# Kernel tuning notes

Measured on AMD Instinct MI355X. Metric: run time of the kernel, lower is better.

## Reference

```python
import jax, jax.numpy as jnp
import numpy as np

B, S, D = 2, 2048, 2048
E, F, TOP_K = 16, 768, 2
NORM_TOPK_PROB = True


def setup_inputs() -> dict:
    key = jax.random.key(0)
    ks = jax.random.split(key, 5)
    sc = 0.02
    return {
        "hidden_states": jax.random.normal(ks[0], (B, S, D), jnp.float32),
        "router_w": jax.random.normal(ks[1], (E, D), jnp.float32) * sc,
        "gate_w": jax.random.normal(ks[2], (E, F, D), jnp.float32) * sc,
        "up_w": jax.random.normal(ks[3], (E, F, D), jnp.float32) * sc,
        "down_w": jax.random.normal(ks[4], (E, D, F), jnp.float32) * sc,
    }


def reference(hidden_states, router_w, gate_w, up_w, down_w):
    b, s, d = hidden_states.shape
    x = hidden_states.reshape(-1, d)                      # [T, D]
    T = x.shape[0]
    # Router: logits, softmax in fp32, top-k
    router_logits = x @ router_w.T                        # [T, E]
    probs = jax.nn.softmax(router_logits.astype(jnp.float32), axis=-1)
    topk_w, topk_idx = jax.lax.top_k(probs, TOP_K)        # [T, K]
    if NORM_TOPK_PROB:
        topk_w = topk_w / jnp.sum(topk_w, axis=-1, keepdims=True)
    topk_w = topk_w.astype(x.dtype)
    # Combine weights as a dense [T, E] matrix (0 for unselected experts);
    # math-equivalent to the per-expert gather/index_add in the original.
    combine = jnp.zeros((T, E), x.dtype).at[jnp.arange(T)[:, None], topk_idx].add(topk_w)
    # Per-expert SwiGLU MLP on all tokens (zero-weight tokens contribute nothing)
    g = jax.nn.silu(jnp.einsum('td,efd->etf', x, gate_w))  # [E, T, F]
    u = jnp.einsum('td,efd->etf', x, up_w)                 # [E, T, F]
    h = (g * u) * combine.T[:, :, None]                    # weight before down-proj
    out = jnp.einsum('etf,edf->td', h, down_w)             # [T, D]
    return out.reshape(b, s, d), router_logits
```

## Files before the change

### kernel.cpp

```cpp
#include <hip/hip_runtime.h>
#include <stdint.h>


#define NTOK 4096
#define DIM  2048
#define NEXP 16
#define FDIM 768
#define BK   32

#define WS_CNT     0
#define WS_CUR     256
#define WS_NTILES  512
#define WS_TILE_E  576
#define WS_TILE_B  736
#define WS_TOKE    1024
#define WS_TOKW    9216
#define WS_SLOTT   17408
#define SLOTW_NEW  27648
#define SLOTW_OLD  26624
#define WS_TOKSLOT 40960
#define MAX_TILES  144

#define TMN 128
#define TNA 64
#define TNB 128
#define MAX_SLOTS_N 10240
#define MAX_TILES_N 80
#define TMO 64
#define MAX_SLOTS_O 9216

#define B_XBF  262144ull
#define B_H    (B_XBF + (size_t)NTOK*DIM*2)
#define B_GBF  (B_H + (size_t)MAX_SLOTS_N*FDIM*2)
#define B_UBF  (B_GBF + (size_t)NEXP*FDIM*DIM*2)
#define B_DBF  (B_UBF + (size_t)NEXP*FDIM*DIM*2)
#define WS_NEED (B_DBF + (size_t)NEXP*FDIM*DIM*2)
#define B_OSL  B_GBF
#define B_HOLD 143360ull

typedef __attribute__((ext_vector_type(8))) short short8;
typedef __attribute__((ext_vector_type(4))) float f32x4;

__device__ __forceinline__ unsigned short f2bf(float f) {
    unsigned u = __float_as_uint(f);
    return (unsigned short)((u + 0x7FFFu + ((u >> 16) & 1u)) >> 16);
}

__device__ __forceinline__ short8 cvt8(float4 v0, float4 v1) {
    short8 s;
    s[0] = (short)f2bf(v0.x); s[1] = (short)f2bf(v0.y);
    s[2] = (short)f2bf(v0.z); s[3] = (short)f2bf(v0.w);
    s[4] = (short)f2bf(v1.x); s[5] = (short)f2bf(v1.y);
    s[6] = (short)f2bf(v1.z); s[7] = (short)f2bf(v1.w);
    return s;
}

__device__ __forceinline__ void gl_lds16(const void* g, void* l) {
    __builtin_amdgcn_global_load_lds(
        (const __attribute__((address_space(1))) unsigned int*)g,
        (__attribute__((address_space(3))) unsigned int*)l, 16, 0, 0);
}

__global__ __launch_bounds__(256) void cvtw_k(
    const float* __restrict__ g, const float* __restrict__ u, const float* __restrict__ d,
    unsigned short* __restrict__ go, unsigned short* __restrict__ uo,
    unsigned short* __restrict__ dd, int n8)
{
    int i = blockIdx.x * 256 + threadIdx.x;
    if (i >= n8) return;
    const float* s;
    unsigned short* o;
    if (blockIdx.y == 0)      { s = g; o = go; }
    else if (blockIdx.y == 1) { s = u; o = uo; }
    else                      { s = d; o = dd; }
    const float4* p = (const float4*)(s + (size_t)i * 8);
    *(short8*)(o + (size_t)i * 8) = cvt8(p[0], p[1]);
}

__global__ __launch_bounds__(256) void router_k(
    const float* __restrict__ x, const float* __restrict__ rw,
    float* __restrict__ logits_out, int* __restrict__ wsi, float* __restrict__ wsf,
    unsigned short* __restrict__ xbf)
{
    int wid = threadIdx.x >> 6, lane = threadIdx.x & 63;
    int t = blockIdx.x * 4 + wid;
    const float* xr = x + (size_t)t * DIM;

    float acc[NEXP];
#pragma unroll
    for (int e = 0; e < NEXP; e++) acc[e] = 0.f;
    for (int i = 0; i < DIM / 64; i++) {
        float xv = xr[i * 64 + lane];
        if (xbf) xbf[(size_t)t * DIM + i * 64 + lane] = f2bf(xv);
#pragma unroll
        for (int e = 0; e < NEXP; e++) acc[e] += xv * rw[e * DIM + i * 64 + lane];
    }
#pragma unroll
    for (int e = 0; e < NEXP; e++) {
        float v = acc[e];
        for (int off = 32; off; off >>= 1) v += __shfl_down(v, off);
        acc[e] = v;
    }
    if (lane == 0) {
#pragma unroll
        for (int e = 0; e < NEXP; e++) logits_out[t * NEXP + e] = acc[e];
        int i0 = 0; float m0 = acc[0];
#pragma unroll
        for (int e = 1; e < NEXP; e++) if (acc[e] > m0) { m0 = acc[e]; i0 = e; }
        int i1 = -1; float m1 = -3.4e38f;
#pragma unroll
        for (int e = 0; e < NEXP; e++) if (e != i0 && acc[e] > m1) { m1 = acc[e]; i1 = e; }
        float w0 = 1.f / (1.f + __expf(m1 - m0));
        wsi[WS_TOKE + t * 2 + 0] = i0;
        wsi[WS_TOKE + t * 2 + 1] = i1;
        wsf[WS_TOKW + t * 2 + 0] = w0;
        wsf[WS_TOKW + t * 2 + 1] = 1.f - w0;
        atomicAdd(&wsi[WS_CNT + i0 * 16], 1);
        atomicAdd(&wsi[WS_CNT + i1 * 16], 1);
    }
}

__global__ void scan_k(int* __restrict__ wsi, float* __restrict__ wsf,
                       int tm, int slotw, int max_slots)
{
    if (threadIdx.x == 0) {
        int total = 0, tiles = 0;
        for (int e = 0; e < NEXP; e++) {
            int c = wsi[WS_CNT + e * 16];
            int nt = (c + tm - 1) / tm;
            wsi[WS_CNT + e * 16] = total;
            for (int j = 0; j < nt; j++) {
                wsi[WS_TILE_E + tiles] = e;
                wsi[WS_TILE_B + tiles] = total + j * tm;
                tiles++;
            }
            total += nt * tm;
        }
        wsi[WS_NTILES] = tiles;
    }
    for (int s = threadIdx.x; s < max_slots; s += blockDim.x) {
        wsi[WS_SLOTT + s] = 0;
        wsf[slotw + s] = 0.f;
    }
}

__global__ __launch_bounds__(256) void scatter_k(int* __restrict__ wsi,
                                                 float* __restrict__ wsf, int slotw)
{
    int t = blockIdx.x * blockDim.x + threadIdx.x;
    if (t >= NTOK) return;
#pragma unroll
    for (int k = 0; k < 2; k++) {
        int e = wsi[WS_TOKE + t * 2 + k];
        float w = wsf[WS_TOKW + t * 2 + k];
        int pos = atomicAdd(&wsi[WS_CUR + e * 16], 1);
        int s = wsi[WS_CNT + e * 16] + pos;
        wsi[WS_SLOTT + s] = t;
        wsf[slotw + s] = w;
        wsi[WS_TOKSLOT + t * 2 + k] = s;
    }
}


__global__ __launch_bounds__(256) void expertA_k(
    const unsigned short* __restrict__ xbf,
    const unsigned short* __restrict__ gbf,
    const unsigned short* __restrict__ ubf,
    const int* __restrict__ wsi, const float* __restrict__ wsf,
    unsigned short* __restrict__ H)
{
    __shared__ union {
        struct {
            unsigned short A[2][TMN * BK];
            unsigned short G[2][TNA * BK];
            unsigned short U[2][TNA * BK];
        } st;
        unsigned short Hs[TMN][TNA + 8];
    } sh;
    __shared__ int   Ts[TMN];
    __shared__ float Wl[TMN];

    int tile = blockIdx.y;
    if (tile >= wsi[WS_NTILES]) return;
    int e     = wsi[WS_TILE_E + tile];
    int slot0 = wsi[WS_TILE_B + tile];
    int f0    = blockIdx.x * TNA;
    int tid   = threadIdx.x;

    if (tid < TMN) {
        Ts[tid] = wsi[WS_SLOTT + slot0 + tid];
        Wl[tid] = wsf[SLOTW_NEW + slot0 + tid];
    }
    __syncthreads();

    int r0 = tid >> 2, seg = tid & 3;
    const unsigned short* ap0 = xbf + (size_t)Ts[r0] * DIM + seg * 8;
    const unsigned short* ap1 = xbf + (size_t)Ts[64 + r0] * DIM + seg * 8;
    const unsigned short* gp  = gbf + ((size_t)e * FDIM + f0 + r0) * DIM + seg * 8;
    const unsigned short* up  = ubf + ((size_t)e * FDIM + f0 + r0) * DIM + seg * 8;

    int wid = tid >> 6, lane = tid & 63;
    int wm = (wid >> 1) * 64, wn = (wid & 1) * 32;
    int lr = lane & 15, lk = (lane >> 4) * 8;

    f32x4 accg[4][2], accu[4][2];
#pragma unroll
    for (int i = 0; i < 4; i++)
#pragma unroll
        for (int j = 0; j < 2; j++) { accg[i][j] = (f32x4)0.f; accu[i][j] = (f32x4)0.f; }

    auto stage = [&](int b, int k0) {
        gl_lds16(ap0 + k0, &sh.st.A[b][(size_t)tid * 8]);
        gl_lds16(ap1 + k0, &sh.st.A[b][(size_t)(256 + tid) * 8]);
        gl_lds16(gp + k0,  &sh.st.G[b][(size_t)tid * 8]);
        gl_lds16(up + k0,  &sh.st.U[b][(size_t)tid * 8]);
    };
    auto comp = [&](int b) {
        short8 a[4], g[2], u[2];
#pragma unroll
        for (int mi = 0; mi < 4; mi++)
            a[mi] = *(const short8*)&sh.st.A[b][(wm + mi * 16 + lr) * BK + lk];
#pragma unroll
        for (int nj = 0; nj < 2; nj++) {
            g[nj] = *(const short8*)&sh.st.G[b][(wn + nj * 16 + lr) * BK + lk];
            u[nj] = *(const short8*)&sh.st.U[b][(wn + nj * 16 + lr) * BK + lk];
        }
#pragma unroll
        for (int mi = 0; mi < 4; mi++)
#pragma unroll
            for (int nj = 0; nj < 2; nj++) {
                accg[mi][nj] = __builtin_amdgcn_mfma_f32_16x16x32_bf16(a[mi], g[nj], accg[mi][nj], 0, 0, 0);
                accu[mi][nj] = __builtin_amdgcn_mfma_f32_16x16x32_bf16(a[mi], u[nj], accu[mi][nj], 0, 0, 0);
            }
    };

    stage(0, 0);
    __syncthreads();
    for (int k0 = 0; k0 < DIM; k0 += 2 * BK) {
        if (k0 + BK < DIM) stage(1, k0 + BK);
        comp(0);
        __syncthreads();
        if (k0 + 2 * BK < DIM) stage(0, k0 + 2 * BK);
        comp(1);
        __syncthreads();
    }

#pragma unroll
    for (int mi = 0; mi < 4; mi++)
#pragma unroll
        for (int nj = 0; nj < 2; nj++)
#pragma unroll
            for (int r = 0; r < 4; r++) {
                int m = wm + mi * 16 + (lane >> 4) * 4 + r;
                int n = wn + nj * 16 + lr;
                float g = accg[mi][nj][r];
                float u = accu[mi][nj][r];
                float sg = g / (1.f + __expf(-g));
                sh.Hs[m][n] = f2bf(sg * u * Wl[m]);
            }
    __syncthreads();

    int row = tid >> 1, cb = (tid & 1) * 32;
    unsigned short* dst = H + (size_t)(slot0 + row) * FDIM + f0 + cb;
#pragma unroll
    for (int c = 0; c < 4; c++)
        *(short8*)(dst + c * 8) = *(const short8*)&sh.Hs[row][cb + c * 8];
}

__global__ __launch_bounds__(256) void expertB_k(
    const unsigned short* __restrict__ H, const unsigned short* __restrict__ dbf,
    const int* __restrict__ wsi, float* __restrict__ O)
{
    __shared__ unsigned short As[2][TMN * BK];
    __shared__ unsigned short Bs[2][TNB * BK];

    int tile = blockIdx.y;
    if (tile >= wsi[WS_NTILES]) return;
    int e     = wsi[WS_TILE_E + tile];
    int slot0 = wsi[WS_TILE_B + tile];
    int d0    = blockIdx.x * TNB;
    int tid   = threadIdx.x;

    int r0 = tid >> 2, seg = tid & 3;
    const unsigned short* ap0 = H + (size_t)(slot0 + r0) * FDIM + seg * 8;
    const unsigned short* ap1 = H + (size_t)(slot0 + 64 + r0) * FDIM + seg * 8;
    const unsigned short* bp0 = dbf + ((size_t)e * DIM + d0 + r0) * FDIM + seg * 8;
    const unsigned short* bp1 = dbf + ((size_t)e * DIM + d0 + 64 + r0) * FDIM + seg * 8;

    int wid = tid >> 6, lane = tid & 63;
    int wm = (wid >> 1) * 64, wn = (wid & 1) * 64;
    int lr = lane & 15, lk = (lane >> 4) * 8;

    f32x4 acc[4][4];
#pragma unroll
    for (int i = 0; i < 4; i++)
#pragma unroll
        for (int j = 0; j < 4; j++) acc[i][j] = (f32x4)0.f;

    auto stage = [&](int b, int k0) {
        gl_lds16(ap0 + k0, &As[b][(size_t)tid * 8]);
        gl_lds16(ap1 + k0, &As[b][(size_t)(256 + tid) * 8]);
        gl_lds16(bp0 + k0, &Bs[b][(size_t)tid * 8]);
        gl_lds16(bp1 + k0, &Bs[b][(size_t)(256 + tid) * 8]);
    };
    auto comp = [&](int bb) {
        short8 a[4], b[4];
#pragma unroll
        for (int i = 0; i < 4; i++) {
            a[i] = *(const short8*)&As[bb][(wm + i * 16 + lr) * BK + lk];
            b[i] = *(const short8*)&Bs[bb][(wn + i * 16 + lr) * BK + lk];
        }
#pragma unroll
        for (int mi = 0; mi < 4; mi++)
#pragma unroll
            for (int nj = 0; nj < 4; nj++)
                acc[mi][nj] = __builtin_amdgcn_mfma_f32_16x16x32_bf16(a[mi], b[nj], acc[mi][nj], 0, 0, 0);
    };

    stage(0, 0);
    __syncthreads();
    for (int k0 = 0; k0 < FDIM; k0 += 2 * BK) {
        if (k0 + BK < FDIM) stage(1, k0 + BK);
        comp(0);
        __syncthreads();
        if (k0 + 2 * BK < FDIM) stage(0, k0 + 2 * BK);
        comp(1);
        __syncthreads();
    }

#pragma unroll
    for (int mi = 0; mi < 4; mi++)
#pragma unroll
        for (int nj = 0; nj < 4; nj++)
#pragma unroll
            for (int r = 0; r < 4; r++) {
                int m = wm + mi * 16 + (lane >> 4) * 4 + r;
                int n = d0 + wn + nj * 16 + lr;
                O[(size_t)(slot0 + m) * DIM + n] = acc[mi][nj][r];
            }
}

__global__ __launch_bounds__(256) void combine_k(
    const float* __restrict__ O, const int* __restrict__ wsi, float* __restrict__ out)
{
    int i = blockIdx.x * 256 + threadIdx.x;
    int t = i >> 9, c = i & 511;
    int s0 = wsi[WS_TOKSLOT + t * 2 + 0];
    int s1 = wsi[WS_TOKSLOT + t * 2 + 1];
    float4 a = *((const float4*)(O + (size_t)s0 * DIM) + c);
    float4 b = *((const float4*)(O + (size_t)s1 * DIM) + c);
    float4 r;
    r.x = a.x + b.x; r.y = a.y + b.y; r.z = a.z + b.z; r.w = a.w + b.w;
    *((float4*)(out + (size_t)t * DIM) + c) = r;
}


__global__ __launch_bounds__(256) void expertA64_k(
    const float* __restrict__ x, const float* __restrict__ gw, const float* __restrict__ uw,
    const int* __restrict__ wsi, const float* __restrict__ wsf,
    unsigned short* __restrict__ H)
{
    __shared__ unsigned short As[TMO][40];
    __shared__ unsigned short Bg[TMO][40];
    __shared__ unsigned short Bu[TMO][40];
    __shared__ unsigned short Hs[TMO][72];
    __shared__ int   Ts[TMO];
    __shared__ float Wl[TMO];

    int tile = blockIdx.y;
    if (tile >= wsi[WS_NTILES]) return;
    int e     = wsi[WS_TILE_E + tile];
    int slot0 = wsi[WS_TILE_B + tile];
    int f0    = blockIdx.x * 64;
    int tid   = threadIdx.x;

    if (tid < TMO) {
        Ts[tid] = wsi[WS_SLOTT + slot0 + tid];
        Wl[tid] = wsf[SLOTW_OLD + slot0 + tid];
    }
    __syncthreads();

    int row = tid >> 2, seg = tid & 3;
    const float* aRow = x  + (size_t)Ts[row] * DIM + seg * 8;
    const float* gRow = gw + ((size_t)e * FDIM + f0 + row) * DIM + seg * 8;
    const float* uRow = uw + ((size_t)e * FDIM + f0 + row) * DIM + seg * 8;

    int wid = tid >> 6, lane = tid & 63;
    int wm = (wid >> 1) * 32, wn = (wid & 1) * 32;
    int lr = lane & 15, lk = (lane >> 4) * 8;

    f32x4 accg[2][2], accu[2][2];
#pragma unroll
    for (int i = 0; i < 2; i++)
#pragma unroll
        for (int j = 0; j < 2; j++) { accg[i][j] = (f32x4)0.f; accu[i][j] = (f32x4)0.f; }

    for (int k0 = 0; k0 < DIM; k0 += BK) {
        { const float4* p = (const float4*)(aRow + k0); *(short8*)&As[row][seg * 8] = cvt8(p[0], p[1]); }
        { const float4* p = (const float4*)(gRow + k0); *(short8*)&Bg[row][seg * 8] = cvt8(p[0], p[1]); }
        { const float4* p = (const float4*)(uRow + k0); *(short8*)&Bu[row][seg * 8] = cvt8(p[0], p[1]); }
        __syncthreads();
        short8 a0 = *(const short8*)&As[wm + lr][lk];
        short8 a1 = *(const short8*)&As[wm + 16 + lr][lk];
        short8 g0 = *(const short8*)&Bg[wn + lr][lk];
        short8 g1 = *(const short8*)&Bg[wn + 16 + lr][lk];
        short8 u0 = *(const short8*)&Bu[wn + lr][lk];
        short8 u1 = *(const short8*)&Bu[wn + 16 + lr][lk];
        accg[0][0] = __builtin_amdgcn_mfma_f32_16x16x32_bf16(a0, g0, accg[0][0], 0, 0, 0);
        accg[0][1] = __builtin_amdgcn_mfma_f32_16x16x32_bf16(a0, g1, accg[0][1], 0, 0, 0);
        accg[1][0] = __builtin_amdgcn_mfma_f32_16x16x32_bf16(a1, g0, accg[1][0], 0, 0, 0);
        accg[1][1] = __builtin_amdgcn_mfma_f32_16x16x32_bf16(a1, g1, accg[1][1], 0, 0, 0);
        accu[0][0] = __builtin_amdgcn_mfma_f32_16x16x32_bf16(a0, u0, accu[0][0], 0, 0, 0);
        accu[0][1] = __builtin_amdgcn_mfma_f32_16x16x32_bf16(a0, u1, accu[0][1], 0, 0, 0);
        accu[1][0] = __builtin_amdgcn_mfma_f32_16x16x32_bf16(a1, u0, accu[1][0], 0, 0, 0);
        accu[1][1] = __builtin_amdgcn_mfma_f32_16x16x32_bf16(a1, u1, accu[1][1], 0, 0, 0);
        __syncthreads();
    }
#pragma unroll
    for (int mi = 0; mi < 2; mi++)
#pragma unroll
        for (int ni = 0; ni < 2; ni++)
#pragma unroll
            for (int r = 0; r < 4; r++) {
                int m = wm + mi * 16 + (lane >> 4) * 4 + r;
                int n = wn + ni * 16 + lr;
                float g = accg[mi][ni][r];
                float u = accu[mi][ni][r];
                Hs[m][n] = f2bf((g / (1.f + __expf(-g))) * u * Wl[m]);
            }
    __syncthreads();
    unsigned short* dst = H + (size_t)(slot0 + row) * FDIM + f0 + seg * 16;
    *(short8*)dst       = *(const short8*)&Hs[row][seg * 16];
    *(short8*)(dst + 8) = *(const short8*)&Hs[row][seg * 16 + 8];
}

__global__ __launch_bounds__(256) void expertB64_k(
    const unsigned short* __restrict__ H, const float* __restrict__ dw,
    const int* __restrict__ wsi, float* __restrict__ out)
{
    __shared__ unsigned short As[TMO][40];
    __shared__ unsigned short Bd[TMO][40];
    __shared__ int Ts[TMO];

    int tile = blockIdx.y;
    if (tile >= wsi[WS_NTILES]) return;
    int e     = wsi[WS_TILE_E + tile];
    int slot0 = wsi[WS_TILE_B + tile];
    int d0    = blockIdx.x * 64;
    int tid   = threadIdx.x;

    if (tid < TMO) Ts[tid] = wsi[WS_SLOTT + slot0 + tid];
    __syncthreads();

    int row = tid >> 2, seg = tid & 3;
    const unsigned short* aRow = H + (size_t)(slot0 + row) * FDIM + seg * 8;
    const float* dRow = dw + ((size_t)e * DIM + d0 + row) * FDIM + seg * 8;

    int wid = tid >> 6, lane = tid & 63;
    int wm = (wid >> 1) * 32, wn = (wid & 1) * 32;
    int lr = lane & 15, lk = (lane >> 4) * 8;

    f32x4 acc[2][2];
#pragma unroll
    for (int i = 0; i < 2; i++)
#pragma unroll
        for (int j = 0; j < 2; j++) acc[i][j] = (f32x4)0.f;

    for (int k0 = 0; k0 < FDIM; k0 += BK) {
        *(short8*)&As[row][seg * 8] = *(const short8*)(aRow + k0);
        { const float4* p = (const float4*)(dRow + k0); *(short8*)&Bd[row][seg * 8] = cvt8(p[0], p[1]); }
        __syncthreads();
        short8 a0 = *(const short8*)&As[wm + lr][lk];
        short8 a1 = *(const short8*)&As[wm + 16 + lr][lk];
        short8 b0 = *(const short8*)&Bd[wn + lr][lk];
        short8 b1 = *(const short8*)&Bd[wn + 16 + lr][lk];
        acc[0][0] = __builtin_amdgcn_mfma_f32_16x16x32_bf16(a0, b0, acc[0][0], 0, 0, 0);
        acc[0][1] = __builtin_amdgcn_mfma_f32_16x16x32_bf16(a0, b1, acc[0][1], 0, 0, 0);
        acc[1][0] = __builtin_amdgcn_mfma_f32_16x16x32_bf16(a1, b0, acc[1][0], 0, 0, 0);
        acc[1][1] = __builtin_amdgcn_mfma_f32_16x16x32_bf16(a1, b1, acc[1][1], 0, 0, 0);
        __syncthreads();
    }
#pragma unroll
    for (int mi = 0; mi < 2; mi++)
#pragma unroll
        for (int ni = 0; ni < 2; ni++)
#pragma unroll
            for (int r = 0; r < 4; r++) {
                int m = wm + mi * 16 + (lane >> 4) * 4 + r;
                int n = d0 + wn + ni * 16 + lr;
                atomicAdd(&out[(size_t)Ts[m] * DIM + n], acc[mi][ni][r]);
            }
}

extern "C" void kernel_launch(void* const* d_in, const int* in_sizes, int n_in,
                              void* d_out, int out_size, void* d_ws, size_t ws_size,
                              hipStream_t stream) {
    const float* x  = (const float*)d_in[0];
    const float* rw = (const float*)d_in[1];
    const float* gw = (const float*)d_in[2];
    const float* uw = (const float*)d_in[3];
    const float* dw = (const float*)d_in[4];
    float* out    = (float*)d_out;
    float* logits = out + (size_t)NTOK * DIM;
    int*   wsi = (int*)d_ws;
    float* wsf = (float*)d_ws;

    hipMemsetAsync(d_ws, 0, 4096, stream);

    if (ws_size >= WS_NEED) {
        unsigned short* xbf = (unsigned short*)((char*)d_ws + B_XBF);
        unsigned short* H   = (unsigned short*)((char*)d_ws + B_H);
        unsigned short* gbf = (unsigned short*)((char*)d_ws + B_GBF);
        unsigned short* ubf = (unsigned short*)((char*)d_ws + B_UBF);
        unsigned short* dbf = (unsigned short*)((char*)d_ws + B_DBF);
        float*          Osl = (float*)((char*)d_ws + B_OSL);
        const int nw8 = NEXP * FDIM * DIM / 8;
        router_k<<<NTOK / 4, 256, 0, stream>>>(x, rw, logits, wsi, wsf, xbf);
        cvtw_k<<<dim3(nw8 / 256, 3), 256, 0, stream>>>(gw, uw, dw, gbf, ubf, dbf, nw8);
        scan_k   <<<1, 256, 0, stream>>>(wsi, wsf, TMN, SLOTW_NEW, MAX_SLOTS_N);
        scatter_k<<<NTOK / 256, 256, 0, stream>>>(wsi, wsf, SLOTW_NEW);
        expertA_k<<<dim3(FDIM / TNA, MAX_TILES_N), 256, 0, stream>>>(xbf, gbf, ubf, wsi, wsf, H);
        expertB_k<<<dim3(DIM / TNB, MAX_TILES_N), 256, 0, stream>>>(H, dbf, wsi, Osl);
        combine_k<<<NTOK * DIM / 4 / 256, 256, 0, stream>>>(Osl, wsi, out);
    } else {
        unsigned short* H = (unsigned short*)((char*)d_ws + B_HOLD);
        hipMemsetAsync(d_out, 0, (size_t)NTOK * DIM * sizeof(float), stream);
        router_k<<<NTOK / 4, 256, 0, stream>>>(x, rw, logits, wsi, wsf, nullptr);
        scan_k   <<<1, 256, 0, stream>>>(wsi, wsf, TMO, SLOTW_OLD, MAX_SLOTS_O);
        scatter_k<<<NTOK / 256, 256, 0, stream>>>(wsi, wsf, SLOTW_OLD);
        expertA64_k<<<dim3(FDIM / 64, MAX_TILES), 256, 0, stream>>>(x, gw, uw, wsi, wsf, H);
        expertB64_k<<<dim3(DIM / 64, MAX_TILES), 256, 0, stream>>>(H, dw, wsi, out);
    }
}
```

Measured before the change: 581.2 us.

## Triple-buffer expert GEMM LDS pipeline with vmcnt waits and MFMA priority

Both expert GEMM kernels move from a double-buffered loop with two __syncthreads per pair of K-steps to a three-stage ring buffer. Loads are issued two stages ahead, and each step waits only for the oldest stage via s_waitcnt vmcnt(4) followed by a single barrier. The aim is to keep more global-to-LDS traffic in flight and cut barrier stalls. s_setprio raises wave priority around the MFMA blocks, and the extra buffer increases LDS use, which may reduce occupancy.

```diff
diff --git a/kernel.cpp b/kernel.cpp
--- a/kernel.cpp
+++ b/kernel.cpp
@@ -171,9 +171,9 @@
 {
     __shared__ union {
         struct {
-            unsigned short A[2][TMN * BK];
-            unsigned short G[2][TNA * BK];
-            unsigned short U[2][TNA * BK];
+            unsigned short A[3][TMN * BK];
+            unsigned short G[3][TNA * BK];
+            unsigned short U[3][TNA * BK];
         } st;
         unsigned short Hs[TMN][TNA + 8];
     } sh;
@@ -225,6 +225,7 @@
             g[nj] = *(const short8*)&sh.st.G[b][(wn + nj * 16 + lr) * BK + lk];
             u[nj] = *(const short8*)&sh.st.U[b][(wn + nj * 16 + lr) * BK + lk];
         }
+        __builtin_amdgcn_s_setprio(1);
 #pragma unroll
         for (int mi = 0; mi < 4; mi++)
 #pragma unroll
@@ -232,18 +233,24 @@
                 accg[mi][nj] = __builtin_amdgcn_mfma_f32_16x16x32_bf16(a[mi], g[nj], accg[mi][nj], 0, 0, 0);
                 accu[mi][nj] = __builtin_amdgcn_mfma_f32_16x16x32_bf16(a[mi], u[nj], accu[mi][nj], 0, 0, 0);
             }
+        __builtin_amdgcn_s_setprio(0);
     };
 
+    const int NS = DIM / BK;
     stage(0, 0);
+    stage(1, BK);
+    int bc = 0, bp = 2;
+    for (int i = 0; i < NS; ++i) {
+        if (i < NS - 1) { asm volatile("s_waitcnt vmcnt(4)" ::: "memory"); }
+        else            { asm volatile("s_waitcnt vmcnt(0)" ::: "memory"); }
+        __builtin_amdgcn_s_barrier();
+        __builtin_amdgcn_sched_barrier(0);
+        if (i + 2 < NS) stage(bp, (i + 2) * BK);
+        comp(bc);
+        bc = (bc == 2) ? 0 : bc + 1;
+        bp = (bp == 2) ? 0 : bp + 1;
+    }
     __syncthreads();
-    for (int k0 = 0; k0 < DIM; k0 += 2 * BK) {
-        if (k0 + BK < DIM) stage(1, k0 + BK);
-        comp(0);
-        __syncthreads();
-        if (k0 + 2 * BK < DIM) stage(0, k0 + 2 * BK);
-        comp(1);
-        __syncthreads();
-    }
 
 #pragma unroll
     for (int mi = 0; mi < 4; mi++)
@@ -271,8 +278,8 @@
     const unsigned short* __restrict__ H, const unsigned short* __restrict__ dbf,
     const int* __restrict__ wsi, float* __restrict__ O)
 {
-    __shared__ unsigned short As[2][TMN * BK];
-    __shared__ unsigned short Bs[2][TNB * BK];
+    __shared__ unsigned short As[3][TMN * BK];
+    __shared__ unsigned short Bs[3][TNB * BK];
 
     int tile = blockIdx.y;
     if (tile >= wsi[WS_NTILES]) return;
@@ -310,22 +317,28 @@
             a[i] = *(const short8*)&As[bb][(wm + i * 16 + lr) * BK + lk];
             b[i] = *(const short8*)&Bs[bb][(wn + i * 16 + lr) * BK + lk];
         }
+        __builtin_amdgcn_s_setprio(1);
 #pragma unroll
         for (int mi = 0; mi < 4; mi++)
 #pragma unroll
             for (int nj = 0; nj < 4; nj++)
                 acc[mi][nj] = __builtin_amdgcn_mfma_f32_16x16x32_bf16(a[mi], b[nj], acc[mi][nj], 0, 0, 0);
+        __builtin_amdgcn_s_setprio(0);
     };
 
+    const int NS = FDIM / BK;
     stage(0, 0);
-    __syncthreads();
-    for (int k0 = 0; k0 < FDIM; k0 += 2 * BK) {
-        if (k0 + BK < FDIM) stage(1, k0 + BK);
-        comp(0);
-        __syncthreads();
-        if (k0 + 2 * BK < FDIM) stage(0, k0 + 2 * BK);
-        comp(1);
-        __syncthreads();
+    stage(1, BK);
+    int bc = 0, bp = 2;
+    for (int i = 0; i < NS; ++i) {
+        if (i < NS - 1) { asm volatile("s_waitcnt vmcnt(4)" ::: "memory"); }
+        else            { asm volatile("s_waitcnt vmcnt(0)" ::: "memory"); }
+        __builtin_amdgcn_s_barrier();
+        __builtin_amdgcn_sched_barrier(0);
+        if (i + 2 < NS) stage(bp, (i + 2) * BK);
+        comp(bc);
+        bc = (bc == 2) ? 0 : bc + 1;
+        bp = (bp == 2) ? 0 : bp + 1;
     }
 
 #pragma unroll
```

Result: no change. 585.4 us (+0.7%).

## Use 256-row expert tiles, single-buffered loads, XCD-aware block swizzle, ballot scatter

Applied to the files above, without the earlier changes.

Expert GEMM tiles grow from 128 to 256 token rows, with narrower N tiles (32 for gate/up, 64 for down). The scan packs pairs of 128-slot chunks into 256-row tiles with a per-tile row count, and partial tiles mask their stores. The LDS double buffering is dropped for a single buffer with a sync per K step. Block indices are remapped so consecutive work lands on the same group of eight (likely per-XCD), and scatter uses wave-aggregated atomics via ballot. The aim is more weight reuse per token tile and better L2 locality, at the cost of lost load/compute overlap and some wasted rows.

```diff
diff --git a/kernel.cpp b/kernel.cpp
--- a/kernel.cpp
+++ b/kernel.cpp
@@ -13,6 +13,7 @@
 #define WS_NTILES  512
 #define WS_TILE_E  576
 #define WS_TILE_B  736
+#define WS_TILE_R  896
 #define WS_TOKE    1024
 #define WS_TOKW    9216
 #define WS_SLOTT   17408
@@ -21,9 +22,9 @@
 #define WS_TOKSLOT 40960
 #define MAX_TILES  144
 
-#define TMN 128
-#define TNA 64
-#define TNB 128
+#define TMN 256
+#define TNA 32
+#define TNB 64
 #define MAX_SLOTS_N 10240
 #define MAX_TILES_N 80
 #define TMO 64
@@ -121,20 +122,38 @@
 }
 
 __global__ void scan_k(int* __restrict__ wsi, float* __restrict__ wsf,
-                       int tm, int slotw, int max_slots)
+                       int mode, int slotw, int max_slots)
 {
     if (threadIdx.x == 0) {
         int total = 0, tiles = 0;
         for (int e = 0; e < NEXP; e++) {
             int c = wsi[WS_CNT + e * 16];
-            int nt = (c + tm - 1) / tm;
             wsi[WS_CNT + e * 16] = total;
-            for (int j = 0; j < nt; j++) {
-                wsi[WS_TILE_E + tiles] = e;
-                wsi[WS_TILE_B + tiles] = total + j * tm;
-                tiles++;
-            }
-            total += nt * tm;
+            if (mode == 1) {
+                int n128 = (c + 127) >> 7;
+                int j = 0;
+                for (; j + 2 <= n128; j += 2) {
+                    wsi[WS_TILE_E + tiles] = e;
+                    wsi[WS_TILE_B + tiles] = total + j * 128;
+                    wsi[WS_TILE_R + tiles] = 256;
+                    tiles++;
+                }
+                if (j < n128) {
+                    wsi[WS_TILE_E + tiles] = e;
+                    wsi[WS_TILE_B + tiles] = total + j * 128;
+                    wsi[WS_TILE_R + tiles] = 128;
+                    tiles++;
+                }
+                total += n128 * 128;
+            } else {
+                int nt = (c + TMO - 1) / TMO;
+                for (int j = 0; j < nt; j++) {
+                    wsi[WS_TILE_E + tiles] = e;
+                    wsi[WS_TILE_B + tiles] = total + j * TMO;
+                    tiles++;
+                }
+                total += nt * TMO;
+            }
         }
         wsi[WS_NTILES] = tiles;
     }
@@ -148,12 +167,23 @@
                                                  float* __restrict__ wsf, int slotw)
 {
     int t = blockIdx.x * blockDim.x + threadIdx.x;
-    if (t >= NTOK) return;
+    int lane = threadIdx.x & 63;
 #pragma unroll
     for (int k = 0; k < 2; k++) {
         int e = wsi[WS_TOKE + t * 2 + k];
         float w = wsf[WS_TOKW + t * 2 + k];
-        int pos = atomicAdd(&wsi[WS_CUR + e * 16], 1);
+        int pos = 0;
+        for (int x = 0; x < NEXP; x++) {
+            unsigned long long mask = __ballot(e == x);
+            if (e == x) {
+                int leader = __ffsll((long long)mask) - 1;
+                int rank = __popcll(mask & ((1ull << lane) - 1ull));
+                int base = 0;
+                if (lane == leader) base = atomicAdd(&wsi[WS_CUR + x * 16], __popcll(mask));
+                base = __shfl(base, leader);
+                pos = base + rank;
+            }
+        }
         int s = wsi[WS_CNT + e * 16] + pos;
         wsi[WS_SLOTT + s] = t;
         wsf[slotw + s] = w;
@@ -171,36 +201,47 @@
 {
     __shared__ union {
         struct {
-            unsigned short A[2][TMN * BK];
-            unsigned short G[2][TNA * BK];
-            unsigned short U[2][TNA * BK];
+            unsigned short A[TMN * BK];
+            unsigned short G[TNA * BK];
+            unsigned short U[TNA * BK];
         } st;
         unsigned short Hs[TMN][TNA + 8];
     } sh;
     __shared__ int   Ts[TMN];
     __shared__ float Wl[TMN];
 
-    int tile = blockIdx.y;
+    int lin  = blockIdx.y * 24 + blockIdx.x;
+    int q    = (24 * MAX_TILES_N) >> 3;
+    int work = (lin & 7) * q + (lin >> 3);
+    int tile = work / 24;
+    int f0   = (work % 24) * TNA;
+
     if (tile >= wsi[WS_NTILES]) return;
     int e     = wsi[WS_TILE_E + tile];
     int slot0 = wsi[WS_TILE_B + tile];
-    int f0    = blockIdx.x * TNA;
+    int rows  = wsi[WS_TILE_R + tile];
     int tid   = threadIdx.x;
 
-    if (tid < TMN) {
-        Ts[tid] = wsi[WS_SLOTT + slot0 + tid];
-        Wl[tid] = wsf[SLOTW_NEW + slot0 + tid];
+    {
+        int s = slot0 + tid;
+        int ok = (s < MAX_SLOTS_N);
+        Ts[tid] = ok ? wsi[WS_SLOTT + s] : 0;
+        Wl[tid] = ok ? wsf[SLOTW_NEW + s] : 0.f;
     }
     __syncthreads();
 
-    int r0 = tid >> 2, seg = tid & 3;
-    const unsigned short* ap0 = xbf + (size_t)Ts[r0] * DIM + seg * 8;
-    const unsigned short* ap1 = xbf + (size_t)Ts[64 + r0] * DIM + seg * 8;
-    const unsigned short* gp  = gbf + ((size_t)e * FDIM + f0 + r0) * DIM + seg * 8;
-    const unsigned short* up  = ubf + ((size_t)e * FDIM + f0 + r0) * DIM + seg * 8;
+    int seg = tid & 3;
+    const unsigned short* ap[4];
+#pragma unroll
+    for (int j = 0; j < 4; j++)
+        ap[j] = xbf + (size_t)Ts[j * 64 + (tid >> 2)] * DIM + seg * 8;
+    const unsigned short* bsrc = (tid < 128 ? gbf : ubf)
+        + ((size_t)e * FDIM + f0 + ((tid & 127) >> 2)) * DIM + seg * 8;
+    unsigned short* bdst = (tid < 128) ? &sh.st.G[(size_t)tid * 8]
+                                       : &sh.st.U[(size_t)(tid - 128) * 8];
 
     int wid = tid >> 6, lane = tid & 63;
-    int wm = (wid >> 1) * 64, wn = (wid & 1) * 32;
+    int wm = wid * 64;
     int lr = lane & 15, lk = (lane >> 4) * 8;
 
     f32x4 accg[4][2], accu[4][2];
@@ -209,21 +250,21 @@
 #pragma unroll
         for (int j = 0; j < 2; j++) { accg[i][j] = (f32x4)0.f; accu[i][j] = (f32x4)0.f; }
 
-    auto stage = [&](int b, int k0) {
-        gl_lds16(ap0 + k0, &sh.st.A[b][(size_t)tid * 8]);
-        gl_lds16(ap1 + k0, &sh.st.A[b][(size_t)(256 + tid) * 8]);
-        gl_lds16(gp + k0,  &sh.st.G[b][(size_t)tid * 8]);
-        gl_lds16(up + k0,  &sh.st.U[b][(size_t)tid * 8]);
-    };
-    auto comp = [&](int b) {
+    for (int k0 = 0; k0 < DIM; k0 += BK) {
+#pragma unroll
+        for (int j = 0; j < 4; j++)
+            gl_lds16(ap[j] + k0, &sh.st.A[(size_t)j * 2048 + (size_t)tid * 8]);
+        gl_lds16(bsrc + k0, bdst);
+        __syncthreads();
+
         short8 a[4], g[2], u[2];
 #pragma unroll
         for (int mi = 0; mi < 4; mi++)
-            a[mi] = *(const short8*)&sh.st.A[b][(wm + mi * 16 + lr) * BK + lk];
+            a[mi] = *(const short8*)&sh.st.A[(wm + mi * 16 + lr) * BK + lk];
 #pragma unroll
         for (int nj = 0; nj < 2; nj++) {
-            g[nj] = *(const short8*)&sh.st.G[b][(wn + nj * 16 + lr) * BK + lk];
-            u[nj] = *(const short8*)&sh.st.U[b][(wn + nj * 16 + lr) * BK + lk];
+            g[nj] = *(const short8*)&sh.st.G[(nj * 16 + lr) * BK + lk];
+            u[nj] = *(const short8*)&sh.st.U[(nj * 16 + lr) * BK + lk];
         }
 #pragma unroll
         for (int mi = 0; mi < 4; mi++)
@@ -232,16 +273,6 @@
                 accg[mi][nj] = __builtin_amdgcn_mfma_f32_16x16x32_bf16(a[mi], g[nj], accg[mi][nj], 0, 0, 0);
                 accu[mi][nj] = __builtin_amdgcn_mfma_f32_16x16x32_bf16(a[mi], u[nj], accu[mi][nj], 0, 0, 0);
             }
-    };
-
-    stage(0, 0);
-    __syncthreads();
-    for (int k0 = 0; k0 < DIM; k0 += 2 * BK) {
-        if (k0 + BK < DIM) stage(1, k0 + BK);
-        comp(0);
-        __syncthreads();
-        if (k0 + 2 * BK < DIM) stage(0, k0 + 2 * BK);
-        comp(1);
         __syncthreads();
     }
 
@@ -252,7 +283,7 @@
 #pragma unroll
             for (int r = 0; r < 4; r++) {
                 int m = wm + mi * 16 + (lane >> 4) * 4 + r;
-                int n = wn + nj * 16 + lr;
+                int n = nj * 16 + lr;
                 float g = accg[mi][nj][r];
                 float u = accu[mi][nj][r];
                 float sg = g / (1.f + __expf(-g));
@@ -260,35 +291,39 @@
             }
     __syncthreads();
 
-    int row = tid >> 1, cb = (tid & 1) * 32;
-    unsigned short* dst = H + (size_t)(slot0 + row) * FDIM + f0 + cb;
-#pragma unroll
-    for (int c = 0; c < 4; c++)
-        *(short8*)(dst + c * 8) = *(const short8*)&sh.Hs[row][cb + c * 8];
+    if (tid < rows) {
+        unsigned short* dst = H + (size_t)(slot0 + tid) * FDIM + f0;
+#pragma unroll
+        for (int c = 0; c < 4; c++)
+            *(short8*)(dst + c * 8) = *(const short8*)&sh.Hs[tid][c * 8];
+    }
 }
 
 __global__ __launch_bounds__(256) void expertB_k(
     const unsigned short* __restrict__ H, const unsigned short* __restrict__ dbf,
     const int* __restrict__ wsi, float* __restrict__ O)
 {
-    __shared__ unsigned short As[2][TMN * BK];
-    __shared__ unsigned short Bs[2][TNB * BK];
-
-    int tile = blockIdx.y;
+    __shared__ unsigned short As[TMN * BK];
+    __shared__ unsigned short Bs[TNB * BK];
+
+    int lin  = blockIdx.y * 32 + blockIdx.x;
+    int q    = (32 * MAX_TILES_N) >> 3;
+    int work = (lin & 7) * q + (lin >> 3);
+    int tile = work >> 5;
+    int d0   = (work & 31) * TNB;
+
     if (tile >= wsi[WS_NTILES]) return;
     int e     = wsi[WS_TILE_E + tile];
     int slot0 = wsi[WS_TILE_B + tile];
-    int d0    = blockIdx.x * TNB;
+    int rows  = wsi[WS_TILE_R + tile];
     int tid   = threadIdx.x;
-
-    int r0 = tid >> 2, seg = tid & 3;
-    const unsigned short* ap0 = H + (size_t)(slot0 + r0) * FDIM + seg * 8;
-    const unsigned short* ap1 = H + (size_t)(slot0 + 64 + r0) * FDIM + seg * 8;
-    const unsigned short* bp0 = dbf + ((size_t)e * DIM + d0 + r0) * FDIM + seg * 8;
-    const unsigned short* bp1 = dbf + ((size_t)e * DIM + d0 + 64 + r0) * FDIM + seg * 8;
+    int seg   = tid & 3;
+
+    const unsigned short* ap = H + (size_t)(slot0 + (tid >> 2)) * FDIM + seg * 8;
+    const unsigned short* bp = dbf + ((size_t)e * DIM + d0 + (tid >> 2)) * FDIM + seg * 8;
 
     int wid = tid >> 6, lane = tid & 63;
-    int wm = (wid >> 1) * 64, wn = (wid & 1) * 64;
+    int wm = wid * 64;
     int lr = lane & 15, lk = (lane >> 4) * 8;
 
     f32x4 acc[4][4];
@@ -297,34 +332,24 @@
 #pragma unroll
         for (int j = 0; j < 4; j++) acc[i][j] = (f32x4)0.f;
 
-    auto stage = [&](int b, int k0) {
-        gl_lds16(ap0 + k0, &As[b][(size_t)tid * 8]);
-        gl_lds16(ap1 + k0, &As[b][(size_t)(256 + tid) * 8]);
-        gl_lds16(bp0 + k0, &Bs[b][(size_t)tid * 8]);
-        gl_lds16(bp1 + k0, &Bs[b][(size_t)(256 + tid) * 8]);
-    };
-    auto comp = [&](int bb) {
+    for (int k0 = 0; k0 < FDIM; k0 += BK) {
+#pragma unroll
+        for (int j = 0; j < 4; j++)
+            gl_lds16(ap + (size_t)j * 64 * FDIM + k0, &As[(size_t)j * 2048 + (size_t)tid * 8]);
+        gl_lds16(bp + k0, &Bs[(size_t)tid * 8]);
+        __syncthreads();
+
         short8 a[4], b[4];
 #pragma unroll
         for (int i = 0; i < 4; i++) {
-            a[i] = *(const short8*)&As[bb][(wm + i * 16 + lr) * BK + lk];
-            b[i] = *(const short8*)&Bs[bb][(wn + i * 16 + lr) * BK + lk];
+            a[i] = *(const short8*)&As[(wm + i * 16 + lr) * BK + lk];
+            b[i] = *(const short8*)&Bs[(i * 16 + lr) * BK + lk];
         }
 #pragma unroll
         for (int mi = 0; mi < 4; mi++)
 #pragma unroll
             for (int nj = 0; nj < 4; nj++)
                 acc[mi][nj] = __builtin_amdgcn_mfma_f32_16x16x32_bf16(a[mi], b[nj], acc[mi][nj], 0, 0, 0);
-    };
-
-    stage(0, 0);
-    __syncthreads();
-    for (int k0 = 0; k0 < FDIM; k0 += 2 * BK) {
-        if (k0 + BK < FDIM) stage(1, k0 + BK);
-        comp(0);
-        __syncthreads();
-        if (k0 + 2 * BK < FDIM) stage(0, k0 + 2 * BK);
-        comp(1);
         __syncthreads();
     }
 
@@ -335,8 +360,10 @@
 #pragma unroll
             for (int r = 0; r < 4; r++) {
                 int m = wm + mi * 16 + (lane >> 4) * 4 + r;
-                int n = d0 + wn + nj * 16 + lr;
-                O[(size_t)(slot0 + m) * DIM + n] = acc[mi][nj][r];
+                if (m < rows) {
+                    int n = d0 + nj * 16 + lr;
+                    O[(size_t)(slot0 + m) * DIM + n] = acc[mi][nj][r];
+                }
             }
 }
 
@@ -517,7 +544,7 @@
         const int nw8 = NEXP * FDIM * DIM / 8;
         router_k<<<NTOK / 4, 256, 0, stream>>>(x, rw, logits, wsi, wsf, xbf);
         cvtw_k<<<dim3(nw8 / 256, 3), 256, 0, stream>>>(gw, uw, dw, gbf, ubf, dbf, nw8);
-        scan_k   <<<1, 256, 0, stream>>>(wsi, wsf, TMN, SLOTW_NEW, MAX_SLOTS_N);
+        scan_k   <<<1, 256, 0, stream>>>(wsi, wsf, 1, SLOTW_NEW, MAX_SLOTS_N);
         scatter_k<<<NTOK / 256, 256, 0, stream>>>(wsi, wsf, SLOTW_NEW);
         expertA_k<<<dim3(FDIM / TNA, MAX_TILES_N), 256, 0, stream>>>(xbf, gbf, ubf, wsi, wsf, H);
         expertB_k<<<dim3(DIM / TNB, MAX_TILES_N), 256, 0, stream>>>(H, dbf, wsi, Osl);
@@ -526,7 +553,7 @@
         unsigned short* H = (unsigned short*)((char*)d_ws + B_HOLD);
         hipMemsetAsync(d_out, 0, (size_t)NTOK * DIM * sizeof(float), stream);
         router_k<<<NTOK / 4, 256, 0, stream>>>(x, rw, logits, wsi, wsf, nullptr);
-        scan_k   <<<1, 256, 0, stream>>>(wsi, wsf, TMO, SLOTW_OLD, MAX_SLOTS_O);
+        scan_k   <<<1, 256, 0, stream>>>(wsi, wsf, 0, SLOTW_OLD, MAX_SLOTS_O);
         scatter_k<<<NTOK / 256, 256, 0, stream>>>(wsi, wsf, SLOTW_OLD);
         expertA64_k<<<dim3(FDIM / 64, MAX_TILES), 256, 0, stream>>>(x, gw, uw, wsi, wsf, H);
         expertB64_k<<<dim3(DIM / 64, MAX_TILES), 256, 0, stream>>>(H, dw, wsi, out);
```

New measurement: 736.9 us. 1.27x slower.
